# Kernel tuning notes

Measured on AMD Instinct MI355X. Metric: run time of the kernel, lower is better.

Reference implementation:

```python
import jax, jax.numpy as jnp
import numpy as np

N, T_PLUS_1, D_IN, WV, HID, V = 64, 33, 1024, 512, 1024, 32000
NULL_IDX = 0


def setup_inputs() -> dict:
    key = jax.random.key(0)
    ks = jax.random.split(key, 9)
    return {
        "features": jax.random.normal(ks[0], (N, D_IN, 4, 4), jnp.float32),
        "captions": jax.random.randint(ks[1], (N, T_PLUS_1), 0, V),
        "W_embed": jax.random.normal(ks[2], (V, WV), jnp.float32) / np.float32(np.sqrt(V)),
        "Wx": jax.random.normal(ks[3], (WV, 4 * HID), jnp.float32) / np.float32(np.sqrt(WV)),
        "Wh": jax.random.normal(ks[4], (HID, 4 * HID), jnp.float32) / np.float32(np.sqrt(HID)),
        "Wattn": jax.random.normal(ks[5], (HID, 4 * HID), jnp.float32) / np.float32(np.sqrt(HID)),
        "b": jnp.zeros((4 * HID,), jnp.float32),
        "W_proj": jax.random.normal(ks[6], (D_IN, HID), jnp.float32) / np.float32(np.sqrt(D_IN)),
        "b_proj": jnp.zeros((HID,), jnp.float32),
        "W_out": jax.random.normal(ks[7], (HID, V), jnp.float32) / np.float32(np.sqrt(HID)),
        "b_out": jnp.zeros((V,), jnp.float32),
    }


def reference(features, captions, W_embed, Wx, Wh, Wattn, b, W_proj, b_proj, W_out, b_out):
    n, _ = captions.shape
    cap_in = captions[:, :-1]   # [N, T]
    cap_out = captions[:, 1:]   # [N, T]

    # project_input applied channel-last: A is [N, H, 4, 4]
    A = jnp.einsum('ndhw,dk->nkhw', features, W_proj) + b_proj[None, :, None, None]
    h0 = A.mean(axis=(2, 3))  # [N, H]
    c0 = h0
    hdim = h0.shape[1]
    A_flat = A.reshape(n, hdim, -1)  # [N, H, P] with P = 16 grid cells
    inv_sqrt_h = jnp.float32(1.0 / np.sqrt(hdim))

    x = W_embed[cap_in]  # [N, T, WV]

    def step(carry, x_t):
        prev_h, prev_c = carry
        # dot-product attention over the spatial grid
        s = jnp.einsum('nh,nhp->np', prev_h, A_flat) * inv_sqrt_h
        w = jax.nn.softmax(s, axis=-1)
        attn = jnp.einsum('nhp,np->nh', A_flat, w)
        # LSTM gating
        a = x_t @ Wx + prev_h @ Wh + attn @ Wattn + b
        i = jax.nn.sigmoid(a[:, :hdim])
        f = jax.nn.sigmoid(a[:, hdim:2 * hdim])
        o = jax.nn.sigmoid(a[:, 2 * hdim:3 * hdim])
        g = jnp.tanh(a[:, 3 * hdim:])
        next_c = f * prev_c + i * g
        next_h = o * jnp.tanh(next_c)
        return (next_h, next_c), next_h

    _, hs = jax.lax.scan(step, (h0, c0), x.transpose(1, 0, 2))  # hs: [T, N, H]
    h = hs.transpose(1, 0, 2)  # [N, T, H]

    scores = h @ W_out + b_out  # [N, T, V]
    logp = jax.nn.log_softmax(scores, axis=-1)
    nll = -jnp.take_along_axis(logp, cap_out[..., None], axis=-1)[..., 0]  # [N, T]
    mask = (cap_out != NULL_IDX).astype(nll.dtype)
    loss = jnp.sum(nll * mask) / n
    return loss
```

## Files before the change

### kernel.cpp

```cpp
#include <hip/hip_runtime.h>
#include <hip/hip_bf16.h>
#include <math.h>

typedef __attribute__((ext_vector_type(8))) short short8;
typedef __attribute__((ext_vector_type(4))) float f32x4;
typedef unsigned short ushort_t;
typedef unsigned int uint_t;

typedef __attribute__((address_space(1))) const void gvoid_t;
typedef __attribute__((address_space(3))) void lvoid_t;

#define VTILES 250

static __device__ __forceinline__ ushort_t f2b(float f){
  __hip_bfloat16 h = __float2bfloat16(f);
  return *reinterpret_cast<ushort_t*>(&h);
}
static __device__ __forceinline__ float b2f(ushort_t u){
  __hip_bfloat16 h = *reinterpret_cast<__hip_bfloat16*>(&u);
  return __bfloat162float(h);
}
static __device__ __forceinline__ float sigmoidf_(float x){ return 1.0f/(1.0f+__expf(-x)); }

__global__ void k_transpose_cvt(const float* __restrict__ src, ushort_t* __restrict__ dst,
                                int C, int dstride, int dcoloff) {
  __shared__ ushort_t tile[64][72];
  int cb = blockIdx.x * 64, rb = blockIdx.y * 64;
  int tid = threadIdx.x;
  for (int it = 0; it < 4; ++it) {
    int e = tid + it*256;
    int row = e >> 4;
    int seg = e & 15;
    float4 v = *reinterpret_cast<const float4*>(&src[(size_t)(rb+row)*C + cb + seg*4]);
    tile[seg*4+0][row] = f2b(v.x);
    tile[seg*4+1][row] = f2b(v.y);
    tile[seg*4+2][row] = f2b(v.z);
    tile[seg*4+3][row] = f2b(v.w);
  }
  __syncthreads();
  for (int it = 0; it < 2; ++it) {
    int e = tid + it*256;
    int cl = e >> 3;
    int seg = e & 7;
    uint4 v = *reinterpret_cast<uint4*>(&tile[cl][seg*8]);
    *reinterpret_cast<uint4*>(&dst[(size_t)(cb+cl)*dstride + dcoloff + rb + seg*8]) = v;
  }
}

__global__ void k_featT(const float* __restrict__ feat, ushort_t* __restrict__ fBT) {
  __shared__ ushort_t t[16][264];
  int n = blockIdx.x;
  int tid = threadIdx.x;
  for (int it = 0; it < 4; ++it) {
    int d = it*256 + tid;
    const float* src = &feat[((size_t)n*1024 + d)*16];
    #pragma unroll
    for (int q = 0; q < 4; ++q) {
      float4 v = *reinterpret_cast<const float4*>(&src[q*4]);
      t[q*4+0][tid] = f2b(v.x);
      t[q*4+1][tid] = f2b(v.y);
      t[q*4+2][tid] = f2b(v.z);
      t[q*4+3][tid] = f2b(v.w);
    }
    __syncthreads();
    #pragma unroll
    for (int w = 0; w < 2; ++w) {
      int e = tid + w*256;
      int p = e >> 5;
      int seg = e & 31;
      uint4 v = *reinterpret_cast<uint4*>(&t[p][seg*8]);
      *reinterpret_cast<uint4*>(&fBT[((size_t)n*16 + p)*1024 + it*256 + seg*8]) = v;
    }
    __syncthreads();
  }
}

__global__ void k_embed(const int* __restrict__ captions, const float* __restrict__ W_embed,
                        ushort_t* __restrict__ xb) {
  int e = (blockIdx.x*256 + threadIdx.x) * 4;
  int nt = e >> 9;
  int n = nt >> 5, t = nt & 31;
  int col = e & 511;
  int tok = captions[n*33 + t];
  float4 v = *reinterpret_cast<const float4*>(&W_embed[(size_t)tok*512 + col]);
  ushort4 o; o.x=f2b(v.x); o.y=f2b(v.y); o.z=f2b(v.z); o.w=f2b(v.w);
  *reinterpret_cast<ushort4*>(&xb[e]) = o;
}

__global__ void k_projmm(const ushort_t* __restrict__ WprojT, const ushort_t* __restrict__ fBT,
                         const float* __restrict__ b_proj, float* __restrict__ A_flat,
                         ushort_t* __restrict__ Abt, float* __restrict__ hbuf) {
  __shared__ ushort_t As[64*64];
  __shared__ ushort_t Bs[64*64];
  int kt = blockIdx.x, nt = blockIdx.y;
  int k0 = kt*64, n0 = nt*64;
  int tid = threadIdx.x;
  int wave = tid>>6, lane = tid&63, lr = lane&15, lg = lane>>4;
  int srow = lane>>3, sxor8 = ((lane&7)^srow)*8;
  f32x4 acc[4];
  #pragma unroll
  for (int nf=0;nf<4;++nf) acc[nf] = (f32x4){0.f,0.f,0.f,0.f};
  for (int kc = 0; kc < 1024; kc += 64){
    __syncthreads();
    #pragma unroll
    for (int u = 0; u < 2; ++u){
      int r0 = wave*16 + u*8;
      const ushort_t* srcA = &WprojT[(size_t)(k0 + r0 + srow)*1024 + kc + sxor8];
      const ushort_t* srcB = &fBT[(size_t)(n0 + r0 + srow)*1024 + kc + sxor8];
      __builtin_amdgcn_global_load_lds((gvoid_t*)srcA, (lvoid_t*)&As[r0*64], 16, 0, 0);
      __builtin_amdgcn_global_load_lds((gvoid_t*)srcB, (lvoid_t*)&Bs[r0*64], 16, 0, 0);
    }
    __syncthreads();
    #pragma unroll
    for (int kk = 0; kk < 2; ++kk){
      int swz = (((kk*4 + lg) ^ (lr & 7)) * 8);
      short8 af = *reinterpret_cast<short8*>(&As[(wave*16 + lr)*64 + swz]);
      #pragma unroll
      for (int nf = 0; nf < 4; ++nf){
        short8 bf = *reinterpret_cast<short8*>(&Bs[(nf*16 + lr)*64 + swz]);
        acc[nf] = __builtin_amdgcn_mfma_f32_16x16x32_bf16(af, bf, acc[nf], 0, 0, 0);
      }
    }
  }
  #pragma unroll
  for (int nf=0;nf<4;++nf){
    int ncol = n0 + nf*16 + lr;
    int nidx = ncol >> 4, p = ncol & 15;
    ushort4 ab;
    #pragma unroll
    for (int r=0;r<4;++r){
      int kh = k0 + wave*16 + lg*4 + r;
      float val = acc[nf][r] + b_proj[kh];
      A_flat[((size_t)nidx*1024 + kh)*16 + p] = val;
      (&ab.x)[r] = f2b(val);
      float s = val;
      s += __shfl_xor(s, 1, 64);
      s += __shfl_xor(s, 2, 64);
      s += __shfl_xor(s, 4, 64);
      s += __shfl_xor(s, 8, 64);
      if (lr == 0) hbuf[(nt*4 + nf)*1024 + kh] = s * (1.f/16.f);
    }
    *reinterpret_cast<ushort4*>(&Abt[(size_t)ncol*1024 + k0 + wave*16 + lg*4]) = ab;
  }
}

__global__ void k_pmm(const ushort_t* __restrict__ WcatT, const ushort_t* __restrict__ Abt,
                      ushort_t* __restrict__ P3) {
  __shared__ ushort_t As[64*64];
  __shared__ ushort_t Bs[64*64];
  __shared__ ushort_t Dt2[64][72];
  int jt = blockIdx.x, nt = blockIdx.y;
  int j0 = jt*64, n0 = nt*64;
  int tid = threadIdx.x;
  int wave = tid>>6, lane = tid&63, lr = lane&15, lg = lane>>4;
  int srow = lane>>3, sxor8 = ((lane&7)^srow)*8;
  f32x4 acc[4];
  #pragma unroll
  for (int nf=0;nf<4;++nf) acc[nf] = (f32x4){0.f,0.f,0.f,0.f};
  for (int kc = 0; kc < 1024; kc += 64){
    __syncthreads();
    #pragma unroll
    for (int u = 0; u < 2; ++u){
      int r0 = wave*16 + u*8;
      const ushort_t* srcA = &WcatT[(size_t)(j0 + r0 + srow)*2560 + 1536 + kc + sxor8];
      const ushort_t* srcB = &Abt[(size_t)(n0 + r0 + srow)*1024 + kc + sxor8];
      __builtin_amdgcn_global_load_lds((gvoid_t*)srcA, (lvoid_t*)&As[r0*64], 16, 0, 0);
      __builtin_amdgcn_global_load_lds((gvoid_t*)srcB, (lvoid_t*)&Bs[r0*64], 16, 0, 0);
    }
    __syncthreads();
    #pragma unroll
    for (int kk = 0; kk < 2; ++kk){
      int swz = (((kk*4 + lg) ^ (lr & 7)) * 8);
      short8 af = *reinterpret_cast<short8*>(&As[(wave*16 + lr)*64 + swz]);
      #pragma unroll
      for (int nf = 0; nf < 4; ++nf){
        short8 bf = *reinterpret_cast<short8*>(&Bs[(nf*16 + lr)*64 + swz]);
        acc[nf] = __builtin_amdgcn_mfma_f32_16x16x32_bf16(af, bf, acc[nf], 0, 0, 0);
      }
    }
  }
  __syncthreads();
  #pragma unroll
  for (int nf=0;nf<4;++nf)
    #pragma unroll
    for (int r=0;r<4;++r)
      Dt2[wave*16 + lg*4 + r][nf*16 + lr] = f2b(acc[nf][r]);
  __syncthreads();
  #pragma unroll
  for (int it=0; it<2; ++it){
    int e = it*256 + tid;
    int row = e >> 3, seg = e & 7;
    uint4 v = *reinterpret_cast<uint4*>(&Dt2[row][seg*8]);
    *reinterpret_cast<uint4*>(&P3[(((size_t)nt*4 + (seg>>1))*4096 + j0 + row)*16 + (seg&1)*8]) = v;
  }
}

__global__ void k_xmm(const ushort_t* __restrict__ WcatT, const ushort_t* __restrict__ xb,
                      ushort_t* __restrict__ xpre) {
  __shared__ ushort_t As[64*64];
  __shared__ ushort_t Bs[64*64];
  __shared__ float Dt[64][68];
  int jt = blockIdx.x, mt = blockIdx.y;
  int j0 = jt*64, m0 = mt*64;
  int tid = threadIdx.x;
  int wave = tid>>6, lane = tid&63, lr = lane&15, lg = lane>>4;
  int srow = lane>>3, sxor8 = ((lane&7)^srow)*8;
  f32x4 acc[4];
  #pragma unroll
  for (int nf=0;nf<4;++nf) acc[nf] = (f32x4){0.f,0.f,0.f,0.f};
  for (int kc = 0; kc < 512; kc += 64){
    __syncthreads();
    #pragma unroll
    for (int u = 0; u < 2; ++u){
      int r0 = wave*16 + u*8;
      const ushort_t* srcA = &WcatT[(size_t)(j0 + r0 + srow)*2560 + kc + sxor8];
      const ushort_t* srcB = &xb[(size_t)(m0 + r0 + srow)*512 + kc + sxor8];
      __builtin_amdgcn_global_load_lds((gvoid_t*)srcA, (lvoid_t*)&As[r0*64], 16, 0, 0);
      __builtin_amdgcn_global_load_lds((gvoid_t*)srcB, (lvoid_t*)&Bs[r0*64], 16, 0, 0);
    }
    __syncthreads();
    #pragma unroll
    for (int kk = 0; kk < 2; ++kk){
      int swz = (((kk*4 + lg) ^ (lr & 7)) * 8);
      short8 af = *reinterpret_cast<short8*>(&As[(wave*16 + lr)*64 + swz]);
      #pragma unroll
      for (int nf = 0; nf < 4; ++nf){
        short8 bf = *reinterpret_cast<short8*>(&Bs[(nf*16 + lr)*64 + swz]);
        acc[nf] = __builtin_amdgcn_mfma_f32_16x16x32_bf16(af, bf, acc[nf], 0, 0, 0);
      }
    }
  }
  __syncthreads();
  #pragma unroll
  for (int nf=0; nf<4; ++nf)
    #pragma unroll
    for (int r=0;r<4;++r)
      Dt[nf*16+lr][wave*16 + lg*4 + r] = acc[nf][r];
  __syncthreads();
  #pragma unroll
  for (int it=0; it<4; ++it){
    int e = tid + it*256;
    int nrow = e >> 4, seg = e & 15;
    float4 v = *reinterpret_cast<float4*>(&Dt[nrow][seg*4]);
    ushort4 o; o.x=f2b(v.x); o.y=f2b(v.y); o.z=f2b(v.z); o.w=f2b(v.w);
    *reinterpret_cast<ushort4*>(&xpre[(size_t)(m0+nrow)*4096 + j0 + seg*4]) = o;
  }
}

__global__ void k_gate(int i, const ushort_t* __restrict__ xpre, const float* __restrict__ a_part,
                       const float* __restrict__ bvec, const ushort_t* __restrict__ P3,
                       const float* __restrict__ A_flat, const float* __restrict__ hbuf,
                       float* __restrict__ cbuf, const float* __restrict__ sp_rd,
                       float* __restrict__ sp_wr, ushort_t* __restrict__ hbf,
                       ushort_t* __restrict__ hall) {
  __shared__ float wvLds[16];
  __shared__ float wred[4][16];
  int n = blockIdx.x >> 2, sp = blockIdx.x & 3;
  int tid = threadIdx.x;
  int wave = tid>>6, lane = tid&63;
  int k = sp*256 + tid;
  float hv;
  if (i == 0){
    hv = hbuf[n*1024 + k];
    cbuf[n*1024 + k] = hv;
    hbf[n*1024 + k] = f2b(hv);
  } else {
    if (tid < 16){
      float sv = (sp_rd[(n*4+0)*16+tid] + sp_rd[(n*4+1)*16+tid] +
                  sp_rd[(n*4+2)*16+tid] + sp_rd[(n*4+3)*16+tid]) * (1.f/32.f);
      float m = sv;
      #pragma unroll
      for (int d=1; d<16; d<<=1) m = fmaxf(m, __shfl_xor(m, d, 64));
      float e = __expf(sv - m);
      float s = e;
      #pragma unroll
      for (int d=1; d<16; d<<=1) s += __shfl_xor(s, d, 64);
      wvLds[tid] = e / s;
    }
    __syncthreads();
    float wv[16];
    #pragma unroll
    for (int p=0;p<16;++p) wv[p] = wvLds[p];
    float av[4];
    #pragma unroll
    for (int g=0;g<4;++g){
      int j = g*1024 + k;
      float x = bvec[j] + b2f(xpre[(size_t)(n*32 + (i-1))*4096 + j]);
      #pragma unroll
      for (int ks=0;ks<8;++ks) x += a_part[((size_t)ks*64 + n)*4096 + j];
      const ushort_t* pp = &P3[((size_t)n*4096 + j)*16];
      short8 p0 = *reinterpret_cast<const short8*>(pp);
      short8 p1 = *reinterpret_cast<const short8*>(pp+8);
      #pragma unroll
      for (int p=0;p<8;++p) x += wv[p]*b2f((ushort_t)p0[p]);
      #pragma unroll
      for (int p=0;p<8;++p) x += wv[8+p]*b2f((ushort_t)p1[p]);
      av[g]=x;
    }
    float ig=sigmoidf_(av[0]), fg=sigmoidf_(av[1]), og=sigmoidf_(av[2]), gg=tanhf(av[3]);
    float c = fg*cbuf[n*1024+k] + ig*gg;
    hv = og*tanhf(c);
    cbuf[n*1024+k] = c;
    hall[((size_t)n*32 + (i-1))*1024 + k] = f2b(hv);
    if (i < 32) hbf[n*1024+k] = f2b(hv);
  }
  if (i == 32) return;
  float sacc[16];
  const float* An = &A_flat[((size_t)n*1024 + k)*16];
  #pragma unroll
  for (int p=0;p<16;p+=4){
    float4 a4 = *reinterpret_cast<const float4*>(&An[p]);
    sacc[p] = hv*a4.x; sacc[p+1] = hv*a4.y; sacc[p+2] = hv*a4.z; sacc[p+3] = hv*a4.w;
  }
  #pragma unroll
  for (int d=1; d<64; d<<=1)
    #pragma unroll
    for (int p=0;p<16;++p) sacc[p] += __shfl_xor(sacc[p], d, 64);
  if (lane == 0)
    #pragma unroll
    for (int p=0;p<16;++p) wred[wave][p] = sacc[p];
  __syncthreads();
  if (tid < 16)
    sp_wr[(n*4+sp)*16 + tid] = wred[0][tid]+wred[1][tid]+wred[2][tid]+wred[3][tid];
}

__global__ void k_mm(const ushort_t* __restrict__ WcatT, const ushort_t* __restrict__ hbf,
                     float* __restrict__ a_part) {
  __shared__ ushort_t As[64*64];
  __shared__ ushort_t Bs[64*64];
  __shared__ float Dt[64][68];
  int jt = blockIdx.x, ks = blockIdx.y;
  int j0 = jt*64;
  int tid = threadIdx.x;
  int wave = tid>>6, lane = tid&63, lr = lane&15, lg = lane>>4;
  int srow = lane>>3, sxor8 = ((lane&7)^srow)*8;
  f32x4 acc[4];
  #pragma unroll
  for (int nf=0;nf<4;++nf) acc[nf] = (f32x4){0.f,0.f,0.f,0.f};
  for (int kc = 0; kc < 128; kc += 64){
    __syncthreads();
    #pragma unroll
    for (int u = 0; u < 2; ++u){
      int r0 = wave*16 + u*8;
      const ushort_t* srcA = &WcatT[(size_t)(j0 + r0 + srow)*2560 + 512 + ks*128 + kc + sxor8];
      const ushort_t* srcB = &hbf[(size_t)(r0 + srow)*1024 + ks*128 + kc + sxor8];
      __builtin_amdgcn_global_load_lds((gvoid_t*)srcA, (lvoid_t*)&As[r0*64], 16, 0, 0);
      __builtin_amdgcn_global_load_lds((gvoid_t*)srcB, (lvoid_t*)&Bs[r0*64], 16, 0, 0);
    }
    __syncthreads();
    #pragma unroll
    for (int kk = 0; kk < 2; ++kk){
      int swz = (((kk*4 + lg) ^ (lr & 7)) * 8);
      short8 af = *reinterpret_cast<short8*>(&As[(wave*16 + lr)*64 + swz]);
      #pragma unroll
      for (int nf = 0; nf < 4; ++nf){
        short8 bf = *reinterpret_cast<short8*>(&Bs[(nf*16 + lr)*64 + swz]);
        acc[nf] = __builtin_amdgcn_mfma_f32_16x16x32_bf16(af, bf, acc[nf], 0, 0, 0);
      }
    }
  }
  __syncthreads();
  #pragma unroll
  for (int nf=0; nf<4; ++nf)
    #pragma unroll
    for (int r=0;r<4;++r)
      Dt[nf*16+lr][wave*16 + lg*4 + r] = acc[nf][r];
  __syncthreads();
  #pragma unroll
  for (int it=0; it<4; ++it){
    int e = tid + it*256;
    int nrow = e >> 4, seg = e & 15;
    float4 v = *reinterpret_cast<float4*>(&Dt[nrow][seg*4]);
    *reinterpret_cast<float4*>(&a_part[((size_t)ks*64 + nrow)*4096 + j0 + seg*4]) = v;
  }
}

__global__ void __launch_bounds__(256, 4)
k_score(const ushort_t* __restrict__ WoutT, const ushort_t* __restrict__ hall,
        const float* __restrict__ b_out,
        float* __restrict__ pmax, float* __restrict__ psum) {
  __shared__ ushort_t As[128*64];
  __shared__ ushort_t Bs[128*64];
  __shared__ float bLds[128];
  __shared__ float pmLds[4][128];
  __shared__ float psLds[4][128];
  int bid = blockIdx.x;
  int wg = (bid & 7) * 500 + (bid >> 3);
  int vb = wg >> 4, rb = wg & 15;
  int v0 = vb * 128, r0 = rb * 128;
  int tid = threadIdx.x;
  int wave = tid >> 6, lane = tid & 63, lr = lane & 15, lg = lane >> 4;
  if (tid < 128) bLds[tid] = b_out[v0 + tid];

  int srow = lane >> 3;
  int sxor = ((lane & 7) ^ srow) << 3;

  f32x4 acc[2][8];
  #pragma unroll
  for (int a=0;a<2;++a)
    #pragma unroll
    for (int q=0;q<8;++q) acc[a][q]=(f32x4){0.f,0.f,0.f,0.f};

  for (int kc = 0; kc < 1024; kc += 64) {
    __syncthreads();
    #pragma unroll
    for (int i = 0; i < 4; ++i) {
      int rowg = (wave*4 + i) * 8;
      const ushort_t* gsA = &WoutT[(size_t)(v0 + rowg + srow)*1024 + kc + sxor];
      const ushort_t* gsB = &hall [(size_t)(r0 + rowg + srow)*1024 + kc + sxor];
      __builtin_amdgcn_global_load_lds((gvoid_t*)gsA, (lvoid_t*)&As[rowg*64], 16, 0, 0);
      __builtin_amdgcn_global_load_lds((gvoid_t*)gsB, (lvoid_t*)&Bs[rowg*64], 16, 0, 0);
    }
    __syncthreads();
    #pragma unroll
    for (int kk = 0; kk < 2; ++kk) {
      int swz = ((kk*4 + lg) ^ (lr & 7)) << 3;
      int rowA = wave*32 + lr;
      short8 af0 = *reinterpret_cast<short8*>(&As[rowA*64 + swz]);
      short8 af1 = *reinterpret_cast<short8*>(&As[(rowA+16)*64 + swz]);
      #pragma unroll
      for (int nr = 0; nr < 8; ++nr) {
        short8 bf = *reinterpret_cast<short8*>(&Bs[(nr*16+lr)*64 + swz]);
        acc[0][nr] = __builtin_amdgcn_mfma_f32_16x16x32_bf16(af0, bf, acc[0][nr], 0,0,0);
        acc[1][nr] = __builtin_amdgcn_mfma_f32_16x16x32_bf16(af1, bf, acc[1][nr], 0,0,0);
      }
    }
  }
  #pragma unroll
  for (int nr=0;nr<8;++nr){
    float m = -1e30f;
    float xv[8];
    #pragma unroll
    for (int mv=0;mv<2;++mv)
      #pragma unroll
      for (int r=0;r<4;++r){
        float x = acc[mv][nr][r] + bLds[wave*32 + mv*16 + lg*4 + r];
        xv[mv*4+r]=x; m = fmaxf(m,x);
      }
    float s=0.f;
    #pragma unroll
    for (int i=0;i<8;++i) s += __expf(xv[i]-m);
    #pragma unroll
    for (int d=16; d<=32; d<<=1){
      float om = __shfl_xor(m, d, 64);
      float os = __shfl_xor(s, d, 64);
      float nm = fmaxf(m, om);
      s = s*__expf(m-nm) + os*__expf(om-nm);
      m = nm;
    }
    if (lg == 0){
      pmLds[wave][nr*16+lr] = m;
      psLds[wave][nr*16+lr] = s;
    }
  }
  __syncthreads();
  if (tid < 128){
    float m=-1e30f;
    #pragma unroll
    for (int w=0;w<4;++w) m = fmaxf(m, pmLds[w][tid]);
    float s=0.f;
    #pragma unroll
    for (int w=0;w<4;++w) s += psLds[w][tid]*__expf(pmLds[w][tid]-m);
    pmax[(size_t)(r0+tid)*VTILES + vb] = m;
    psum[(size_t)(r0+tid)*VTILES + vb] = s;
  }
}

__global__ void k_tgt(const ushort_t* __restrict__ hall, const ushort_t* __restrict__ WoutT,
                      const float* __restrict__ b_out, const int* __restrict__ captions,
                      float* __restrict__ stgt) {
  int tid = threadIdx.x;
  int wave = tid>>6, lane = tid&63;
  int r = blockIdx.x*4 + wave;
  int n = r>>5, t = r&31;
  int y = captions[n*33 + t + 1];
  const ushort_t* hrow = hall + (size_t)r*1024;
  const ushort_t* wrow = WoutT + (size_t)y*1024;
  float dot = 0.f;
  #pragma unroll
  for (int i=0;i<2;++i){
    int off = lane*8 + i*512;
    short8 hv = *reinterpret_cast<const short8*>(&hrow[off]);
    short8 wv = *reinterpret_cast<const short8*>(&wrow[off]);
    #pragma unroll
    for (int e2=0;e2<8;++e2) dot += b2f((ushort_t)hv[e2])*b2f((ushort_t)wv[e2]);
  }
  #pragma unroll
  for (int d=32; d>=1; d>>=1) dot += __shfl_xor(dot, d, 64);
  if (lane==0) stgt[r] = dot + b_out[y];
}

__global__ void k_reduce(const float* __restrict__ pmax, const float* __restrict__ psum,
                         const float* __restrict__ stgt, const int* __restrict__ captions,
                         float* __restrict__ row_loss) {
  int tid = threadIdx.x;
  int wave = tid>>6, lane = tid&63;
  int r = blockIdx.x*4 + wave;
  float m = -1e30f, s = 0.f;
  for (int j = lane; j < VTILES; j += 64){
    float mj = pmax[(size_t)r*VTILES + j];
    float sj = psum[(size_t)r*VTILES + j];
    float nm = fmaxf(m, mj);
    s = s*__expf(m-nm) + sj*__expf(mj-nm);
    m = nm;
  }
  #pragma unroll
  for (int d=32; d>=1; d>>=1){
    float om = __shfl_xor(m, d, 64);
    float os = __shfl_xor(s, d, 64);
    float nm = fmaxf(m, om);
    s = s*__expf(m-nm) + os*__expf(om-nm);
    m = nm;
  }
  if (lane==0){
    int n = r>>5, t = r&31;
    int y = captions[n*33 + t + 1];
    float lse = m + __logf(s);
    row_loss[r] = (y != 0) ? (lse - stgt[r]) : 0.f;
  }
}

__global__ void k_final(const float* __restrict__ row_loss, float* __restrict__ out) {
  __shared__ float red[256];
  int tid = threadIdx.x;
  float s = 0.f;
  #pragma unroll
  for (int i=0;i<8;++i) s += row_loss[tid + i*256];
  red[tid] = s;
  __syncthreads();
  for (int off=128; off>=1; off>>=1){
    if (tid<off) red[tid] += red[tid+off];
    __syncthreads();
  }
  if (tid==0) out[0] = red[0] * (1.f/64.f);
}

extern "C" void kernel_launch(void* const* d_in, const int* in_sizes, int n_in,
                              void* d_out, int out_size, void* d_ws, size_t ws_size,
                              hipStream_t stream) {
  const float* features = (const float*)d_in[0];
  const int*   captions = (const int*)d_in[1];
  const float* W_embed  = (const float*)d_in[2];
  const float* Wx       = (const float*)d_in[3];
  const float* Wh       = (const float*)d_in[4];
  const float* Wattn    = (const float*)d_in[5];
  const float* b        = (const float*)d_in[6];
  const float* W_proj   = (const float*)d_in[7];
  const float* b_proj   = (const float*)d_in[8];
  const float* W_out    = (const float*)d_in[9];
  const float* b_out    = (const float*)d_in[10];
  float* out = (float*)d_out;

  char* wsp = (char*)d_ws;
  size_t off = 0;
  auto alloc = [&](size_t bytes)->char*{
    char* p = wsp + off; off += (bytes + 255) & ~(size_t)255; return p;
  };
  ushort_t* WcatT  = (ushort_t*)alloc((size_t)4096*2560*2);
  ushort_t* WoutT  = (ushort_t*)alloc((size_t)32000*1024*2);
  ushort_t* WprojT = (ushort_t*)alloc((size_t)1024*1024*2);
  ushort_t* fBT    = (ushort_t*)alloc((size_t)1024*1024*2);
  ushort_t* Abt    = (ushort_t*)alloc((size_t)1024*1024*2);
  float* A_flat    = (float*)alloc((size_t)64*1024*16*4);
  ushort_t* xb     = (ushort_t*)alloc((size_t)64*32*512*2);
  float* hbuf      = (float*)alloc((size_t)64*1024*4);
  ushort_t* P3     = (ushort_t*)alloc((size_t)64*4096*16*2);
  ushort_t* xpre   = (ushort_t*)alloc((size_t)2048*4096*2);
  float* a_part    = (float*)alloc((size_t)8*64*4096*4);
  ushort_t* hbf    = (ushort_t*)alloc((size_t)64*1024*2);
  float* cbuf      = (float*)alloc((size_t)64*1024*4);
  float* spbuf     = (float*)alloc((size_t)2*64*4*16*4);
  ushort_t* hall   = (ushort_t*)alloc((size_t)2048*1024*2);
  float* pmax      = (float*)alloc((size_t)2048*250*4);
  float* psum      = (float*)alloc((size_t)2048*250*4);
  float* stgt      = (float*)alloc((size_t)2048*4);
  float* row_loss  = (float*)alloc((size_t)2048*4);

  hipLaunchKernelGGL(k_transpose_cvt, dim3(64, 8),   dim3(256), 0, stream, Wx,     WcatT,  4096, 2560, 0);
  hipLaunchKernelGGL(k_transpose_cvt, dim3(64, 16),  dim3(256), 0, stream, Wh,     WcatT,  4096, 2560, 512);
  hipLaunchKernelGGL(k_transpose_cvt, dim3(64, 16),  dim3(256), 0, stream, Wattn,  WcatT,  4096, 2560, 1536);
  hipLaunchKernelGGL(k_transpose_cvt, dim3(500, 16), dim3(256), 0, stream, W_out,  WoutT,  32000, 1024, 0);
  hipLaunchKernelGGL(k_transpose_cvt, dim3(16, 16),  dim3(256), 0, stream, W_proj, WprojT, 1024, 1024, 0);
  hipLaunchKernelGGL(k_featT, dim3(64), dim3(256), 0, stream, features, fBT);
  hipLaunchKernelGGL(k_embed, dim3(1024), dim3(256), 0, stream, captions, W_embed, xb);
  hipLaunchKernelGGL(k_projmm, dim3(16, 16), dim3(256), 0, stream, WprojT, fBT, b_proj, A_flat, Abt, hbuf);
  hipLaunchKernelGGL(k_pmm, dim3(64, 16), dim3(256), 0, stream, WcatT, Abt, P3);
  hipLaunchKernelGGL(k_xmm, dim3(64, 32), dim3(256), 0, stream, WcatT, xb, xpre);

  for (int i = 0; i <= 32; ++i){
    const float* sp_rd = spbuf + ((i+1)&1)*4096;
    float*       sp_wr = spbuf + (i&1)*4096;
    hipLaunchKernelGGL(k_gate, dim3(256), dim3(256), 0, stream, i, xpre, a_part, b, P3,
                       A_flat, hbuf, cbuf, sp_rd, sp_wr, hbf, hall);
    if (i < 32)
      hipLaunchKernelGGL(k_mm, dim3(64, 8), dim3(256), 0, stream, WcatT, hbf, a_part);
  }

  hipLaunchKernelGGL(k_score, dim3(4000), dim3(256), 0, stream, WoutT, hall, b_out, pmax, psum);
  hipLaunchKernelGGL(k_tgt, dim3(512), dim3(256), 0, stream, hall, WoutT, b_out, captions, stgt);
  hipLaunchKernelGGL(k_reduce, dim3(512), dim3(256), 0, stream, pmax, psum, stgt, captions, row_loss);
  hipLaunchKernelGGL(k_final, dim3(1), dim3(256), 0, stream, row_loss, out);
}
```

Before: 673.1 us.

## Fuse LSTM gate and recurrent matmul into one launch with flag sync

The per-step gate kernel and the recurrent h·Wh matmul kernel are merged into one launch with 768 blocks. The first 256 blocks compute the gates and publish a per-block step counter with a release store. The remaining 512 blocks prefetch their Wh tile into LDS, then spin on those counters before loading h and running the MFMA matmul. This removes one kernel boundary per timestep and overlaps the weight prefetch with the gate computation, at the cost of spin-waiting and a reliance on all 768 blocks being co-resident. Separately, the target-logit kernel and the log-sum-exp reduction kernel are fused into one kernel, dropping an intermediate buffer and a launch.

```diff
diff --git a/kernel.cpp b/kernel.cpp
--- a/kernel.cpp
+++ b/kernel.cpp
@@ -247,131 +247,164 @@
   }
 }
 
-__global__ void k_gate(int i, const ushort_t* __restrict__ xpre, const float* __restrict__ a_part,
-                       const float* __restrict__ bvec, const ushort_t* __restrict__ P3,
-                       const float* __restrict__ A_flat, const float* __restrict__ hbuf,
-                       float* __restrict__ cbuf, const float* __restrict__ sp_rd,
-                       float* __restrict__ sp_wr, ushort_t* __restrict__ hbf,
-                       ushort_t* __restrict__ hall) {
+__global__ void __launch_bounds__(256, 4)
+k_step(int i, const ushort_t* __restrict__ xpre, float* __restrict__ a_part,
+       const float* __restrict__ bvec, const ushort_t* __restrict__ P3,
+       const float* __restrict__ A_flat, const float* __restrict__ hbuf,
+       float* __restrict__ cbuf, const float* __restrict__ sp_rd,
+       float* __restrict__ sp_wr, ushort_t* __restrict__ hbf,
+       ushort_t* __restrict__ hall, const ushort_t* __restrict__ WcatT,
+       uint_t* __restrict__ done) {
+  __shared__ char smem[32768];
   __shared__ float wvLds[16];
   __shared__ float wred[4][16];
-  int n = blockIdx.x >> 2, sp = blockIdx.x & 3;
+  int b = blockIdx.x;
   int tid = threadIdx.x;
   int wave = tid>>6, lane = tid&63;
-  int k = sp*256 + tid;
-  float hv;
-  if (i == 0){
-    hv = hbuf[n*1024 + k];
-    cbuf[n*1024 + k] = hv;
-    hbf[n*1024 + k] = f2b(hv);
+  int srow = lane>>3, sxor8 = ((lane&7)^srow)*8;
+
+  if (b < 256) {
+    int n = b >> 2, sp = b & 3;
+    int k = sp*256 + tid;
+    float hv;
+    if (i == 0){
+      hv = hbuf[n*1024 + k];
+      cbuf[n*1024 + k] = hv;
+      hbf[n*1024 + k] = f2b(hv);
+    } else {
+      if (tid < 16){
+        float sv = (sp_rd[(n*4+0)*16+tid] + sp_rd[(n*4+1)*16+tid] +
+                    sp_rd[(n*4+2)*16+tid] + sp_rd[(n*4+3)*16+tid]) * (1.f/32.f);
+        float m = sv;
+        #pragma unroll
+        for (int d=1; d<16; d<<=1) m = fmaxf(m, __shfl_xor(m, d, 64));
+        float e = __expf(sv - m);
+        float s = e;
+        #pragma unroll
+        for (int d=1; d<16; d<<=1) s += __shfl_xor(s, d, 64);
+        wvLds[tid] = e / s;
+      }
+      __syncthreads();
+      float wv[16];
+      #pragma unroll
+      for (int p=0;p<16;++p) wv[p] = wvLds[p];
+      float av[4];
+      #pragma unroll
+      for (int g=0;g<4;++g){
+        int j = g*1024 + k;
+        float x = bvec[j] + b2f(xpre[(size_t)(n*32 + (i-1))*4096 + j]);
+        #pragma unroll
+        for (int ks=0;ks<8;++ks) x += a_part[((size_t)ks*64 + n)*4096 + j];
+        const ushort_t* pp = &P3[((size_t)n*4096 + j)*16];
+        short8 p0 = *reinterpret_cast<const short8*>(pp);
+        short8 p1 = *reinterpret_cast<const short8*>(pp+8);
+        #pragma unroll
+        for (int p=0;p<8;++p) x += wv[p]*b2f((ushort_t)p0[p]);
+        #pragma unroll
+        for (int p=0;p<8;++p) x += wv[8+p]*b2f((ushort_t)p1[p]);
+        av[g]=x;
+      }
+      float ig=sigmoidf_(av[0]), fg=sigmoidf_(av[1]), og=sigmoidf_(av[2]), gg=tanhf(av[3]);
+      float c = fg*cbuf[n*1024+k] + ig*gg;
+      hv = og*tanhf(c);
+      cbuf[n*1024+k] = c;
+      hall[((size_t)n*32 + (i-1))*1024 + k] = f2b(hv);
+      if (i < 32) hbf[n*1024+k] = f2b(hv);
+    }
+    if (i < 32){
+      __syncthreads();
+      if (tid == 0){
+        __threadfence();
+        __hip_atomic_store(&done[b], (uint_t)(i+1), __ATOMIC_RELEASE, __HIP_MEMORY_SCOPE_AGENT);
+      }
+    }
+    if (i == 32) return;
+    float sacc[16];
+    const float* An = &A_flat[((size_t)n*1024 + k)*16];
+    #pragma unroll
+    for (int p=0;p<16;p+=4){
+      float4 a4 = *reinterpret_cast<const float4*>(&An[p]);
+      sacc[p] = hv*a4.x; sacc[p+1] = hv*a4.y; sacc[p+2] = hv*a4.z; sacc[p+3] = hv*a4.w;
+    }
+    #pragma unroll
+    for (int d=1; d<64; d<<=1)
+      #pragma unroll
+      for (int p=0;p<16;++p) sacc[p] += __shfl_xor(sacc[p], d, 64);
+    if (lane == 0)
+      #pragma unroll
+      for (int p=0;p<16;++p) wred[wave][p] = sacc[p];
+    __syncthreads();
+    if (tid < 16)
+      sp_wr[(n*4+sp)*16 + tid] = wred[0][tid]+wred[1][tid]+wred[2][tid]+wred[3][tid];
   } else {
-    if (tid < 16){
-      float sv = (sp_rd[(n*4+0)*16+tid] + sp_rd[(n*4+1)*16+tid] +
-                  sp_rd[(n*4+2)*16+tid] + sp_rd[(n*4+3)*16+tid]) * (1.f/32.f);
-      float m = sv;
-      #pragma unroll
-      for (int d=1; d<16; d<<=1) m = fmaxf(m, __shfl_xor(m, d, 64));
-      float e = __expf(sv - m);
-      float s = e;
-      #pragma unroll
-      for (int d=1; d<16; d<<=1) s += __shfl_xor(s, d, 64);
-      wvLds[tid] = e / s;
-    }
-    __syncthreads();
-    float wv[16];
-    #pragma unroll
-    for (int p=0;p<16;++p) wv[p] = wvLds[p];
-    float av[4];
-    #pragma unroll
-    for (int g=0;g<4;++g){
-      int j = g*1024 + k;
-      float x = bvec[j] + b2f(xpre[(size_t)(n*32 + (i-1))*4096 + j]);
-      #pragma unroll
-      for (int ks=0;ks<8;++ks) x += a_part[((size_t)ks*64 + n)*4096 + j];
-      const ushort_t* pp = &P3[((size_t)n*4096 + j)*16];
-      short8 p0 = *reinterpret_cast<const short8*>(pp);
-      short8 p1 = *reinterpret_cast<const short8*>(pp+8);
-      #pragma unroll
-      for (int p=0;p<8;++p) x += wv[p]*b2f((ushort_t)p0[p]);
-      #pragma unroll
-      for (int p=0;p<8;++p) x += wv[8+p]*b2f((ushort_t)p1[p]);
-      av[g]=x;
-    }
-    float ig=sigmoidf_(av[0]), fg=sigmoidf_(av[1]), og=sigmoidf_(av[2]), gg=tanhf(av[3]);
-    float c = fg*cbuf[n*1024+k] + ig*gg;
-    hv = og*tanhf(c);
-    cbuf[n*1024+k] = c;
-    hall[((size_t)n*32 + (i-1))*1024 + k] = f2b(hv);
-    if (i < 32) hbf[n*1024+k] = f2b(hv);
-  }
-  if (i == 32) return;
-  float sacc[16];
-  const float* An = &A_flat[((size_t)n*1024 + k)*16];
-  #pragma unroll
-  for (int p=0;p<16;p+=4){
-    float4 a4 = *reinterpret_cast<const float4*>(&An[p]);
-    sacc[p] = hv*a4.x; sacc[p+1] = hv*a4.y; sacc[p+2] = hv*a4.z; sacc[p+3] = hv*a4.w;
-  }
-  #pragma unroll
-  for (int d=1; d<64; d<<=1)
-    #pragma unroll
-    for (int p=0;p<16;++p) sacc[p] += __shfl_xor(sacc[p], d, 64);
-  if (lane == 0)
-    #pragma unroll
-    for (int p=0;p<16;++p) wred[wave][p] = sacc[p];
-  __syncthreads();
-  if (tid < 16)
-    sp_wr[(n*4+sp)*16 + tid] = wred[0][tid]+wred[1][tid]+wred[2][tid]+wred[3][tid];
-}
-
-__global__ void k_mm(const ushort_t* __restrict__ WcatT, const ushort_t* __restrict__ hbf,
-                     float* __restrict__ a_part) {
-  __shared__ ushort_t As[64*64];
-  __shared__ ushort_t Bs[64*64];
-  __shared__ float Dt[64][68];
-  int jt = blockIdx.x, ks = blockIdx.y;
-  int j0 = jt*64;
-  int tid = threadIdx.x;
-  int wave = tid>>6, lane = tid&63, lr = lane&15, lg = lane>>4;
-  int srow = lane>>3, sxor8 = ((lane&7)^srow)*8;
-  f32x4 acc[4];
-  #pragma unroll
-  for (int nf=0;nf<4;++nf) acc[nf] = (f32x4){0.f,0.f,0.f,0.f};
-  for (int kc = 0; kc < 128; kc += 64){
-    __syncthreads();
-    #pragma unroll
-    for (int u = 0; u < 2; ++u){
-      int r0 = wave*16 + u*8;
-      const ushort_t* srcA = &WcatT[(size_t)(j0 + r0 + srow)*2560 + 512 + ks*128 + kc + sxor8];
-      const ushort_t* srcB = &hbf[(size_t)(r0 + srow)*1024 + ks*128 + kc + sxor8];
-      __builtin_amdgcn_global_load_lds((gvoid_t*)srcA, (lvoid_t*)&As[r0*64], 16, 0, 0);
-      __builtin_amdgcn_global_load_lds((gvoid_t*)srcB, (lvoid_t*)&Bs[r0*64], 16, 0, 0);
-    }
-    __syncthreads();
-    #pragma unroll
-    for (int kk = 0; kk < 2; ++kk){
-      int swz = (((kk*4 + lg) ^ (lr & 7)) * 8);
-      short8 af = *reinterpret_cast<short8*>(&As[(wave*16 + lr)*64 + swz]);
-      #pragma unroll
-      for (int nf = 0; nf < 4; ++nf){
-        short8 bf = *reinterpret_cast<short8*>(&Bs[(nf*16 + lr)*64 + swz]);
-        acc[nf] = __builtin_amdgcn_mfma_f32_16x16x32_bf16(af, bf, acc[nf], 0, 0, 0);
-      }
-    }
-  }
-  __syncthreads();
-  #pragma unroll
-  for (int nf=0; nf<4; ++nf)
-    #pragma unroll
-    for (int r=0;r<4;++r)
-      Dt[nf*16+lr][wave*16 + lg*4 + r] = acc[nf][r];
-  __syncthreads();
-  #pragma unroll
-  for (int it=0; it<4; ++it){
-    int e = tid + it*256;
-    int nrow = e >> 4, seg = e & 15;
-    float4 v = *reinterpret_cast<float4*>(&Dt[nrow][seg*4]);
-    *reinterpret_cast<float4*>(&a_part[((size_t)ks*64 + nrow)*4096 + j0 + seg*4]) = v;
+    ushort_t* AsL = reinterpret_cast<ushort_t*>(smem);
+    ushort_t* BsL = reinterpret_cast<ushort_t*>(smem + 16384);
+    int idx = b - 256;
+    int jt = idx & 63, ks = idx >> 6;
+    int j0 = jt*64;
+    #pragma unroll
+    for (int c = 0; c < 2; ++c)
+      #pragma unroll
+      for (int u = 0; u < 2; ++u){
+        int r0 = wave*16 + u*8;
+        const ushort_t* srcA = &WcatT[(size_t)(j0 + r0 + srow)*2560 + 512 + ks*128 + c*64 + sxor8];
+        __builtin_amdgcn_global_load_lds((gvoid_t*)srcA, (lvoid_t*)&AsL[(c*64 + r0)*64], 16, 0, 0);
+      }
+    if (wave == 0){
+      const uint_t tgt = (uint_t)(i+1);
+      for (;;){
+        bool ok = true;
+        #pragma unroll
+        for (int q=0;q<4;++q){
+          uint_t v = __hip_atomic_load(&done[lane*4+q], __ATOMIC_RELAXED, __HIP_MEMORY_SCOPE_AGENT);
+          ok &= (v >= tgt);
+        }
+        if (__all(ok)) break;
+        __builtin_amdgcn_s_sleep(1);
+      }
+    }
+    __syncthreads();
+    __threadfence();
+    #pragma unroll
+    for (int c = 0; c < 2; ++c)
+      #pragma unroll
+      for (int u = 0; u < 2; ++u){
+        int r0 = wave*16 + u*8;
+        const ushort_t* srcB = &hbf[(size_t)(r0 + srow)*1024 + ks*128 + c*64 + sxor8];
+        __builtin_amdgcn_global_load_lds((gvoid_t*)srcB, (lvoid_t*)&BsL[(c*64 + r0)*64], 16, 0, 0);
+      }
+    int lr = lane & 15, lg = lane >> 4;
+    f32x4 acc[4];
+    #pragma unroll
+    for (int nf=0;nf<4;++nf) acc[nf] = (f32x4){0.f,0.f,0.f,0.f};
+    __syncthreads();
+    #pragma unroll
+    for (int c = 0; c < 2; ++c)
+      #pragma unroll
+      for (int kk = 0; kk < 2; ++kk){
+        int swz = (((kk*4 + lg) ^ (lr & 7)) * 8);
+        short8 af = *reinterpret_cast<short8*>(&AsL[(c*64 + wave*16 + lr)*64 + swz]);
+        #pragma unroll
+        for (int nf = 0; nf < 4; ++nf){
+          short8 bf = *reinterpret_cast<short8*>(&BsL[(c*64 + nf*16 + lr)*64 + swz]);
+          acc[nf] = __builtin_amdgcn_mfma_f32_16x16x32_bf16(af, bf, acc[nf], 0, 0, 0);
+        }
+      }
+    __syncthreads();
+    float (*Dt)[68] = reinterpret_cast<float(*)[68]>(smem);
+    #pragma unroll
+    for (int nf=0; nf<4; ++nf)
+      #pragma unroll
+      for (int r=0;r<4;++r)
+        Dt[nf*16+lr][wave*16 + lg*4 + r] = acc[nf][r];
+    __syncthreads();
+    #pragma unroll
+    for (int it=0; it<4; ++it){
+      int e = tid + it*256;
+      int nrow = e >> 4, seg = e & 15;
+      float4 v = *reinterpret_cast<float4*>(&Dt[nrow][seg*4]);
+      *reinterpret_cast<float4*>(&a_part[((size_t)ks*64 + nrow)*4096 + j0 + seg*4]) = v;
+    }
   }
 }
 
@@ -466,9 +499,10 @@
   }
 }
 
-__global__ void k_tgt(const ushort_t* __restrict__ hall, const ushort_t* __restrict__ WoutT,
+__global__ void k_nll(const ushort_t* __restrict__ hall, const ushort_t* __restrict__ WoutT,
                       const float* __restrict__ b_out, const int* __restrict__ captions,
-                      float* __restrict__ stgt) {
+                      const float* __restrict__ pmax, const float* __restrict__ psum,
+                      float* __restrict__ row_loss) {
   int tid = threadIdx.x;
   int wave = tid>>6, lane = tid&63;
   int r = blockIdx.x*4 + wave;
@@ -485,17 +519,6 @@
     #pragma unroll
     for (int e2=0;e2<8;++e2) dot += b2f((ushort_t)hv[e2])*b2f((ushort_t)wv[e2]);
   }
-  #pragma unroll
-  for (int d=32; d>=1; d>>=1) dot += __shfl_xor(dot, d, 64);
-  if (lane==0) stgt[r] = dot + b_out[y];
-}
-
-__global__ void k_reduce(const float* __restrict__ pmax, const float* __restrict__ psum,
-                         const float* __restrict__ stgt, const int* __restrict__ captions,
-                         float* __restrict__ row_loss) {
-  int tid = threadIdx.x;
-  int wave = tid>>6, lane = tid&63;
-  int r = blockIdx.x*4 + wave;
   float m = -1e30f, s = 0.f;
   for (int j = lane; j < VTILES; j += 64){
     float mj = pmax[(size_t)r*VTILES + j];
@@ -506,6 +529,7 @@
   }
   #pragma unroll
   for (int d=32; d>=1; d>>=1){
+    dot += __shfl_xor(dot, d, 64);
     float om = __shfl_xor(m, d, 64);
     float os = __shfl_xor(s, d, 64);
     float nm = fmaxf(m, om);
@@ -513,10 +537,8 @@
     m = nm;
   }
   if (lane==0){
-    int n = r>>5, t = r&31;
-    int y = captions[n*33 + t + 1];
     float lse = m + __logf(s);
-    row_loss[r] = (y != 0) ? (lse - stgt[r]) : 0.f;
+    row_loss[r] = (y != 0) ? (lse - (dot + b_out[y])) : 0.f;
   }
 }
 
@@ -573,8 +595,10 @@
   ushort_t* hall   = (ushort_t*)alloc((size_t)2048*1024*2);
   float* pmax      = (float*)alloc((size_t)2048*250*4);
   float* psum      = (float*)alloc((size_t)2048*250*4);
-  float* stgt      = (float*)alloc((size_t)2048*4);
   float* row_loss  = (float*)alloc((size_t)2048*4);
+  uint_t* done     = (uint_t*)alloc((size_t)256*4);
+
+  hipMemsetAsync(done, 0, 256*4, stream);
 
   hipLaunchKernelGGL(k_transpose_cvt, dim3(64, 8),   dim3(256), 0, stream, Wx,     WcatT,  4096, 2560, 0);
   hipLaunchKernelGGL(k_transpose_cvt, dim3(64, 16),  dim3(256), 0, stream, Wh,     WcatT,  4096, 2560, 512);
@@ -590,14 +614,12 @@
   for (int i = 0; i <= 32; ++i){
     const float* sp_rd = spbuf + ((i+1)&1)*4096;
     float*       sp_wr = spbuf + (i&1)*4096;
-    hipLaunchKernelGGL(k_gate, dim3(256), dim3(256), 0, stream, i, xpre, a_part, b, P3,
-                       A_flat, hbuf, cbuf, sp_rd, sp_wr, hbf, hall);
-    if (i < 32)
-      hipLaunchKernelGGL(k_mm, dim3(64, 8), dim3(256), 0, stream, WcatT, hbf, a_part);
+    hipLaunchKernelGGL(k_step, dim3(i < 32 ? 768 : 256), dim3(256), 0, stream,
+                       i, xpre, a_part, b, P3, A_flat, hbuf, cbuf, sp_rd, sp_wr,
+                       hbf, hall, WcatT, done);
   }
 
   hipLaunchKernelGGL(k_score, dim3(4000), dim3(256), 0, stream, WoutT, hall, b_out, pmax, psum);
-  hipLaunchKernelGGL(k_tgt, dim3(512), dim3(256), 0, stream, hall, WoutT, b_out, captions, stgt);
-  hipLaunchKernelGGL(k_reduce, dim3(512), dim3(256), 0, stream, pmax, psum, stgt, captions, row_loss);
+  hipLaunchKernelGGL(k_nll, dim3(512), dim3(256), 0, stream, hall, WoutT, b_out, captions, pmax, psum, row_loss);
   hipLaunchKernelGGL(k_final, dim3(1), dim3(256), 0, stream, row_loss, out);
 }
```

Result: slower. 2.133 ms (+216.9%).

## Rewrite score GEMM with 256x128 tiles, triple-buffered LDS pipeline, fuse target/reduce kernels

Applied to the files above, without the earlier changes.

The vocabulary-score GEMM moves from 128x128 tiles with 4 waves and a single LDS buffer to 256x128 tiles with 8 waves. Global-to-LDS loads are triple-buffered, and prefetches are interleaved with MFMA phases under explicit waitcnt, barriers and setprio. This halves the number of vocabulary tiles, so the partial log-sum-exp buffers shrink. The target-logit dot product and the row reduction are merged into one kernel, removing a launch and an intermediate buffer. In exchange, LDS use per block is much larger and the manual scheduling must be exactly right.

```diff
diff --git a/kernel.cpp b/kernel.cpp
--- a/kernel.cpp
+++ b/kernel.cpp
@@ -10,7 +10,7 @@
 typedef __attribute__((address_space(1))) const void gvoid_t;
 typedef __attribute__((address_space(3))) void lvoid_t;
 
-#define VTILES 250
+#define VTILES 125
 
 static __device__ __forceinline__ ushort_t f2b(float f){
   __hip_bfloat16 h = __float2bfloat16(f);
@@ -375,100 +375,162 @@
   }
 }
 
-__global__ void __launch_bounds__(256, 4)
+__global__ void __launch_bounds__(512, 2)
 k_score(const ushort_t* __restrict__ WoutT, const ushort_t* __restrict__ hall,
         const float* __restrict__ b_out,
         float* __restrict__ pmax, float* __restrict__ psum) {
-  __shared__ ushort_t As[128*64];
-  __shared__ ushort_t Bs[128*64];
-  __shared__ float bLds[128];
-  __shared__ float pmLds[4][128];
-  __shared__ float psLds[4][128];
+  __shared__ ushort_t A_lds[3][16384];
+  __shared__ ushort_t B_lds[3][8192];
+  __shared__ float bLds[256];
+  __shared__ float pmLds[2][128];
+  __shared__ float psLds[2][128];
+
   int bid = blockIdx.x;
-  int wg = (bid & 7) * 500 + (bid >> 3);
+  int wg = (bid & 7) * 250 + (bid >> 3);
   int vb = wg >> 4, rb = wg & 15;
-  int v0 = vb * 128, r0 = rb * 128;
-  int tid = threadIdx.x;
-  int wave = tid >> 6, lane = tid & 63, lr = lane & 15, lg = lane >> 4;
-  if (tid < 128) bLds[tid] = b_out[v0 + tid];
-
-  int srow = lane >> 3;
-  int sxor = ((lane & 7) ^ srow) << 3;
-
-  f32x4 acc[2][8];
-  #pragma unroll
-  for (int a=0;a<2;++a)
-    #pragma unroll
-    for (int q=0;q<8;++q) acc[a][q]=(f32x4){0.f,0.f,0.f,0.f};
-
-  for (int kc = 0; kc < 1024; kc += 64) {
-    __syncthreads();
-    #pragma unroll
-    for (int i = 0; i < 4; ++i) {
-      int rowg = (wave*4 + i) * 8;
-      const ushort_t* gsA = &WoutT[(size_t)(v0 + rowg + srow)*1024 + kc + sxor];
-      const ushort_t* gsB = &hall [(size_t)(r0 + rowg + srow)*1024 + kc + sxor];
-      __builtin_amdgcn_global_load_lds((gvoid_t*)gsA, (lvoid_t*)&As[rowg*64], 16, 0, 0);
-      __builtin_amdgcn_global_load_lds((gvoid_t*)gsB, (lvoid_t*)&Bs[rowg*64], 16, 0, 0);
-    }
-    __syncthreads();
-    #pragma unroll
-    for (int kk = 0; kk < 2; ++kk) {
-      int swz = ((kk*4 + lg) ^ (lr & 7)) << 3;
-      int rowA = wave*32 + lr;
-      short8 af0 = *reinterpret_cast<short8*>(&As[rowA*64 + swz]);
-      short8 af1 = *reinterpret_cast<short8*>(&As[(rowA+16)*64 + swz]);
-      #pragma unroll
-      for (int nr = 0; nr < 8; ++nr) {
-        short8 bf = *reinterpret_cast<short8*>(&Bs[(nr*16+lr)*64 + swz]);
-        acc[0][nr] = __builtin_amdgcn_mfma_f32_16x16x32_bf16(af0, bf, acc[0][nr], 0,0,0);
-        acc[1][nr] = __builtin_amdgcn_mfma_f32_16x16x32_bf16(af1, bf, acc[1][nr], 0,0,0);
-      }
-    }
-  }
-  #pragma unroll
-  for (int nr=0;nr<8;++nr){
+  size_t v0 = (size_t)vb * 256, r0 = (size_t)rb * 128;
+  int tid = threadIdx.x;
+  int wid = tid >> 6, lane = tid & 63;
+  int wr = wid >> 2, wc = wid & 3;
+  int lr = lane & 15, lg = lane >> 4;
+  int srow = lane >> 3, sxor8 = ((lane & 7) ^ srow) * 8;
+
+  const ushort_t* Abase = WoutT + v0*1024 + (size_t)srow*1024 + sxor8;
+  const ushort_t* Bbase = hall  + r0*1024 + (size_t)srow*1024 + sxor8;
+
+  auto stA = [&](int set, int u, int t){
+    __builtin_amdgcn_global_load_lds(
+      (gvoid_t*)(Abase + (size_t)(u*64 + wid*8)*1024 + t*64),
+      (lvoid_t*)&A_lds[set][(u*64 + wid*8)*64], 16, 0, 0);
+  };
+  auto stB = [&](int set, int u, int t){
+    __builtin_amdgcn_global_load_lds(
+      (gvoid_t*)(Bbase + (size_t)(u*64 + wid*8)*1024 + t*64),
+      (lvoid_t*)&B_lds[set][(u*64 + wid*8)*64], 16, 0, 0);
+  };
+
+  f32x4 acc[8][2];
+  #pragma unroll
+  for (int fi=0; fi<8; ++fi)
+    #pragma unroll
+    for (int fj=0; fj<2; ++fj) acc[fi][fj] = (f32x4){0.f,0.f,0.f,0.f};
+
+  short8 afr[4][2], bfr[2][2];
+  auto ldA = [&](int set, int qv){
+    #pragma unroll
+    for (int f=0; f<4; ++f)
+      #pragma unroll
+      for (int kk=0; kk<2; ++kk){
+        int row = wr*128 + (qv*4+f)*16 + lr;
+        afr[f][kk] = *reinterpret_cast<short8*>(&A_lds[set][row*64 + (((kk*4+lg)^(lr&7))*8)]);
+      }
+  };
+  auto ldB = [&](int set){
+    #pragma unroll
+    for (int fj=0; fj<2; ++fj)
+      #pragma unroll
+      for (int kk=0; kk<2; ++kk){
+        int row = wc*32 + fj*16 + lr;
+        bfr[fj][kk] = *reinterpret_cast<short8*>(&B_lds[set][row*64 + (((kk*4+lg)^(lr&7))*8)]);
+      }
+  };
+  auto mfma16 = [&](int qv){
+    __builtin_amdgcn_s_setprio(1);
+    #pragma unroll
+    for (int f=0; f<4; ++f)
+      #pragma unroll
+      for (int fj=0; fj<2; ++fj)
+        #pragma unroll
+        for (int kk=0; kk<2; ++kk)
+          acc[qv*4+f][fj] = __builtin_amdgcn_mfma_f32_16x16x32_bf16(
+              afr[f][kk], bfr[fj][kk], acc[qv*4+f][fj], 0, 0, 0);
+    __builtin_amdgcn_s_setprio(0);
+  };
+
+  stA(0,0,0); stA(0,1,0); stA(0,2,0); stA(0,3,0); stB(0,0,0); stB(0,1,0);
+  stA(1,0,1); stA(1,1,1); stA(1,2,1); stA(1,3,1); stB(1,0,1); stB(1,1,1);
+  asm volatile("s_waitcnt vmcnt(6)" ::: "memory");
+  __builtin_amdgcn_s_barrier();
+  __builtin_amdgcn_sched_barrier(0);
+
+  for (int g = 0; g < 16; ++g){
+    int s = g % 3, sn = (g + 2) % 3;
+    int tn = g + 2;
+    bool st = tn < 16;
+    ldA(s, 0); ldB(s);
+    if (st){ stA(sn,0,tn); stA(sn,1,tn); stA(sn,2,tn); }
+    __builtin_amdgcn_sched_barrier(0);
+    __builtin_amdgcn_s_barrier();
+    __builtin_amdgcn_sched_barrier(0);
+    mfma16(0);
+    __builtin_amdgcn_sched_barrier(0);
+    __builtin_amdgcn_s_barrier();
+    __builtin_amdgcn_sched_barrier(0);
+    ldA(s, 1);
+    if (st){ stA(sn,3,tn); stB(sn,0,tn); stB(sn,1,tn); }
+    if (g == 14)      { asm volatile("s_waitcnt vmcnt(0)" ::: "memory"); }
+    else if (g < 14)  { asm volatile("s_waitcnt vmcnt(6)" ::: "memory"); }
+    __builtin_amdgcn_sched_barrier(0);
+    __builtin_amdgcn_s_barrier();
+    __builtin_amdgcn_sched_barrier(0);
+    mfma16(1);
+    __builtin_amdgcn_sched_barrier(0);
+    __builtin_amdgcn_s_barrier();
+    __builtin_amdgcn_sched_barrier(0);
+  }
+
+  if (tid < 256) bLds[tid] = b_out[v0 + tid];
+  __syncthreads();
+  float pm_[2], ps_[2];
+  #pragma unroll
+  for (int fj=0; fj<2; ++fj){
     float m = -1e30f;
-    float xv[8];
-    #pragma unroll
-    for (int mv=0;mv<2;++mv)
-      #pragma unroll
-      for (int r=0;r<4;++r){
-        float x = acc[mv][nr][r] + bLds[wave*32 + mv*16 + lg*4 + r];
-        xv[mv*4+r]=x; m = fmaxf(m,x);
-      }
-    float s=0.f;
-    #pragma unroll
-    for (int i=0;i<8;++i) s += __expf(xv[i]-m);
+    #pragma unroll
+    for (int fi=0; fi<8; ++fi)
+      #pragma unroll
+      for (int rr=0; rr<4; ++rr){
+        float x = acc[fi][fj][rr] + bLds[wr*128 + fi*16 + lg*4 + rr];
+        m = fmaxf(m, x);
+      }
+    float ssum = 0.f;
+    #pragma unroll
+    for (int fi=0; fi<8; ++fi)
+      #pragma unroll
+      for (int rr=0; rr<4; ++rr){
+        float x = acc[fi][fj][rr] + bLds[wr*128 + fi*16 + lg*4 + rr];
+        ssum += __expf(x - m);
+      }
     #pragma unroll
     for (int d=16; d<=32; d<<=1){
       float om = __shfl_xor(m, d, 64);
-      float os = __shfl_xor(s, d, 64);
+      float os = __shfl_xor(ssum, d, 64);
       float nm = fmaxf(m, om);
-      s = s*__expf(m-nm) + os*__expf(om-nm);
+      ssum = ssum*__expf(m-nm) + os*__expf(om-nm);
       m = nm;
     }
-    if (lg == 0){
-      pmLds[wave][nr*16+lr] = m;
-      psLds[wave][nr*16+lr] = s;
+    pm_[fj] = m; ps_[fj] = ssum;
+  }
+  if (lg == 0){
+    #pragma unroll
+    for (int fj=0; fj<2; ++fj){
+      pmLds[wr][wc*32 + fj*16 + lr] = pm_[fj];
+      psLds[wr][wc*32 + fj*16 + lr] = ps_[fj];
     }
   }
   __syncthreads();
   if (tid < 128){
-    float m=-1e30f;
-    #pragma unroll
-    for (int w=0;w<4;++w) m = fmaxf(m, pmLds[w][tid]);
-    float s=0.f;
-    #pragma unroll
-    for (int w=0;w<4;++w) s += psLds[w][tid]*__expf(pmLds[w][tid]-m);
-    pmax[(size_t)(r0+tid)*VTILES + vb] = m;
-    psum[(size_t)(r0+tid)*VTILES + vb] = s;
-  }
-}
-
-__global__ void k_tgt(const ushort_t* __restrict__ hall, const ushort_t* __restrict__ WoutT,
+    float m0 = pmLds[0][tid], m1 = pmLds[1][tid];
+    float m = fmaxf(m0, m1);
+    float sv = psLds[0][tid]*__expf(m0-m) + psLds[1][tid]*__expf(m1-m);
+    pmax[(size_t)(r0 + tid)*VTILES + vb] = m;
+    psum[(size_t)(r0 + tid)*VTILES + vb] = sv;
+  }
+}
+
+__global__ void k_nll(const ushort_t* __restrict__ hall, const ushort_t* __restrict__ WoutT,
                       const float* __restrict__ b_out, const int* __restrict__ captions,
-                      float* __restrict__ stgt) {
+                      const float* __restrict__ pmax, const float* __restrict__ psum,
+                      float* __restrict__ row_loss) {
   int tid = threadIdx.x;
   int wave = tid>>6, lane = tid&63;
   int r = blockIdx.x*4 + wave;
@@ -485,17 +547,6 @@
     #pragma unroll
     for (int e2=0;e2<8;++e2) dot += b2f((ushort_t)hv[e2])*b2f((ushort_t)wv[e2]);
   }
-  #pragma unroll
-  for (int d=32; d>=1; d>>=1) dot += __shfl_xor(dot, d, 64);
-  if (lane==0) stgt[r] = dot + b_out[y];
-}
-
-__global__ void k_reduce(const float* __restrict__ pmax, const float* __restrict__ psum,
-                         const float* __restrict__ stgt, const int* __restrict__ captions,
-                         float* __restrict__ row_loss) {
-  int tid = threadIdx.x;
-  int wave = tid>>6, lane = tid&63;
-  int r = blockIdx.x*4 + wave;
   float m = -1e30f, s = 0.f;
   for (int j = lane; j < VTILES; j += 64){
     float mj = pmax[(size_t)r*VTILES + j];
@@ -506,6 +557,7 @@
   }
   #pragma unroll
   for (int d=32; d>=1; d>>=1){
+    dot += __shfl_xor(dot, d, 64);
     float om = __shfl_xor(m, d, 64);
     float os = __shfl_xor(s, d, 64);
     float nm = fmaxf(m, om);
@@ -513,10 +565,8 @@
     m = nm;
   }
   if (lane==0){
-    int n = r>>5, t = r&31;
-    int y = captions[n*33 + t + 1];
     float lse = m + __logf(s);
-    row_loss[r] = (y != 0) ? (lse - stgt[r]) : 0.f;
+    row_loss[r] = (y != 0) ? (lse - (dot + b_out[y])) : 0.f;
   }
 }
 
@@ -571,9 +621,8 @@
   float* cbuf      = (float*)alloc((size_t)64*1024*4);
   float* spbuf     = (float*)alloc((size_t)2*64*4*16*4);
   ushort_t* hall   = (ushort_t*)alloc((size_t)2048*1024*2);
-  float* pmax      = (float*)alloc((size_t)2048*250*4);
-  float* psum      = (float*)alloc((size_t)2048*250*4);
-  float* stgt      = (float*)alloc((size_t)2048*4);
+  float* pmax      = (float*)alloc((size_t)2048*VTILES*4);
+  float* psum      = (float*)alloc((size_t)2048*VTILES*4);
   float* row_loss  = (float*)alloc((size_t)2048*4);
 
   hipLaunchKernelGGL(k_transpose_cvt, dim3(64, 8),   dim3(256), 0, stream, Wx,     WcatT,  4096, 2560, 0);
@@ -596,8 +645,7 @@
       hipLaunchKernelGGL(k_mm, dim3(64, 8), dim3(256), 0, stream, WcatT, hbf, a_part);
   }
 
-  hipLaunchKernelGGL(k_score, dim3(4000), dim3(256), 0, stream, WoutT, hall, b_out, pmax, psum);
-  hipLaunchKernelGGL(k_tgt, dim3(512), dim3(256), 0, stream, hall, WoutT, b_out, captions, stgt);
-  hipLaunchKernelGGL(k_reduce, dim3(512), dim3(256), 0, stream, pmax, psum, stgt, captions, row_loss);
+  hipLaunchKernelGGL(k_score, dim3(2000), dim3(512), 0, stream, WoutT, hall, b_out, pmax, psum);
+  hipLaunchKernelGGL(k_nll, dim3(512), dim3(256), 0, stream, hall, WoutT, b_out, captions, pmax, psum, row_loss);
   hipLaunchKernelGGL(k_final, dim3(1), dim3(256), 0, stream, row_loss, out);
 }
```

Measured after the change: 673.8 us. No clear change (+0.1%).
